# Performance work log

Hardware: AMD Instinct MI355X
Metric: run time of the kernel (lower is better)

The kernel has to match this reference:

```python
import jax, jax.numpy as jnp
import numpy as np
from jax import lax

B = 16   # batch
A = 40   # num_attributes

def _conv(x, w, b, pad):
    y = lax.conv_general_dilated(x, w, (1, 1), [(pad, pad), (pad, pad)],
                                 dimension_numbers=('NCHW', 'OIHW', 'NCHW'))
    return y + b[None, :, None, None]

def _bn_relu(y):
    # BatchNorm2d in training mode; gamma=1, beta=0 (the module's init values)
    m = y.mean(axis=(0, 2, 3), keepdims=True)
    v = ((y - m) ** 2).mean(axis=(0, 2, 3), keepdims=True)
    return jax.nn.relu((y - m) * lax.rsqrt(v + 1e-5))

def _maxpool2(y):
    return lax.reduce_window(y, -jnp.inf, lax.max, (1, 1, 2, 2), (1, 1, 2, 2), 'VALID')

def _gsm(s, t):
    # gumbel_softmax(s, t) == softmax(s / t) along dim 1 (no noise in source)
    return jax.nn.softmax(s / t, axis=1)

def _branch_layer(xb, wa, ba, wb, bb, br, t):
    # xb: [P, B, Cin, H, W]; wa/wb: per-branch conv weights stacked on axis 0
    def one(x, wai, bai, wbi, bbi):
        y = _bn_relu(_conv(x, wai, bai, 1))
        y = _bn_relu(_conv(y, wbi, bbi, 1))
        return _maxpool2(y)
    xs = jax.vmap(one)(xb, wa, ba, wb, bb)       # [P, B, Cout, H/2, W/2]
    # branching_op (training=True): d = softmax(log(softmax(br/0.5)) / t)
    d = _gsm(jnp.log(_gsm(br, 0.5)), float(t))   # [Cnext, P]
    return jnp.einsum('np,pbchw->nbchw', d, xs)  # weighted sum over parents

def reference(x, w10, b10, wa0, ba0, wb0, bb0, wa1, ba1, wb1, bb1,
              wa2, ba2, wb2, bb2, wa3, ba3, wb3, bb3,
              br0, br1, br2, br3, fw1, fb1, fw2, fb2, fw3, fb3, t):
    y = _maxpool2(_bn_relu(_conv(x, w10, b10, 0)))   # conv1_0: [B,64,125,125]
    xb = jnp.stack([y, y])                           # x_branches = [x, x]
    for wa, ba, wb, bb, br in ((wa0, ba0, wb0, bb0, br0),
                               (wa1, ba1, wb1, bb1, br1),
                               (wa2, ba2, wb2, bb2, br2),
                               (wa3, ba3, wb3, bb3, br3)):
        xb = _branch_layer(xb, wa, ba, wb, bb, br, t)
    # xb: [A, B, 32, 7, 7]; AdaptiveAvgPool2d((7,7)) on 7x7 input is identity
    f = xb.reshape(A, B, -1)                          # [A, B, 1568]
    # per-attribute fc1/fc2 heads batched over the attribute axis (dropout omitted)
    h = jax.nn.relu(jnp.einsum('abf,afh->abh', f, fw1) + fb1[:, None, :])
    h = jax.nn.relu(jnp.einsum('abh,ahk->abk', h, fw2) + fb2[:, None, :])
    o = jnp.einsum('abh,ahk->abk', h, fw3) + fb3[:, None, :]   # [A, B, 1]
    return jnp.transpose(o[:, :, 0])                  # cat along dim 1 -> [B, A]

def setup_inputs():
    key = jax.random.key(0)
    ki = iter(jax.random.split(key, 64))
    def rn(shape, s):
        return jax.random.normal(next(ki), shape, jnp.float32) * s
    inp = {'x': jax.random.normal(next(ki), (B, 3, 256, 256), jnp.float32)}
    inp['w10'] = rn((64, 3, 7, 7), 0.1)
    inp['b10'] = jnp.zeros((64,), jnp.float32)
    P = [2, 4, 8, 16]       # parents per branch layer
    cout = [64, 64, 64, 32] # num_in_channels[layer+1]
    for L in range(4):
        inp['wa%d' % L] = rn((P[L], 64, 64, 3, 3), 0.06)
        inp['ba%d' % L] = jnp.zeros((P[L], 64), jnp.float32)
        inp['wb%d' % L] = rn((P[L], cout[L], 64, 3, 3), 0.06)
        inp['bb%d' % L] = jnp.zeros((P[L], cout[L]), jnp.float32)
    C = [4, 8, 16, A]       # children per branch layer
    for L in range(4):
        inp['br%d' % L] = jax.random.uniform(next(ki), (C[L], P[L]), dtype=jnp.float32)
    inp['fw1'] = rn((A, 1568, 128), 0.01)
    inp['fb1'] = jnp.zeros((A, 128), jnp.float32)
    inp['fw2'] = rn((A, 128, 128), 0.01)
    inp['fb2'] = jnp.zeros((A, 128), jnp.float32)
    inp['fw3'] = rn((A, 128, 1), 0.01)
    inp['fb3'] = jnp.zeros((A, 1), jnp.float32)
    inp['t'] = 10
    return inp
```

## Files before the change

### kernel.cpp

```cpp
#include <hip/hip_runtime.h>
#include <math.h>

#define DIVUP(a,b) (((a)+(b)-1)/(b))

typedef _Float16 f16x8 __attribute__((ext_vector_type(8)));
typedef _Float16 f16x4 __attribute__((ext_vector_type(4)));
typedef float    f32x4 __attribute__((ext_vector_type(4)));

#define LBAR() do { asm volatile("s_waitcnt lgkmcnt(0)" ::: "memory"); \
                    __builtin_amdgcn_s_barrier(); } while (0)

template<int POOL, int C1, int HinP, int WinP, int Hout, int Wout, int Cout,
         int M, int NITER, int H2, int W2, int H2c, int W2c>
__global__ __launch_bounds__(256, 4) void conv_mfma(
    const _Float16* __restrict__ in, long inZstride,
    const _Float16* __restrict__ wt,
    float* __restrict__ out, long outZstride, float2* __restrict__ part)
{
    __shared__ __align__(16) char smem[10240];
    float2* red = (float2*)smem;

    int bx;
    {
        int n = gridDim.x, orig = blockIdx.x;
        int q = n >> 3, r = n & 7;
        int xcd = orig & 7, idx = orig >> 3;
        bx = (xcd < r ? xcd * (q + 1) : r * (q + 1) + (xcd - r) * q) + idx;
    }

    const int tid  = threadIdx.x;
    const int wv   = tid >> 6;
    const int ln15 = tid & 15;
    const int lhi  = (tid >> 4) & 3;
    const int sn   = tid & 63;
    const int skb  = tid >> 6;
    const int sdst = sn * 40 + skb * 8;

    const _Float16* ip = in + (size_t)blockIdx.z * inZstride;

    auto pixbase = [&](int mA) -> int {
        int nb, h, w; bool valid;
        if (POOL) {
            int r = mA & 3, quad = mA >> 2;
            const int cpi = H2c * W2c;
            nb = quad / cpi;
            int rem = quad - nb * cpi;
            int h2 = rem / W2c, w2 = rem - h2 * W2c;
            h = h2 * 2 + (r >> 1); w = w2 * 2 + (r & 1);
            valid = (mA < M) && (h < Hout) && (w < Wout);
        } else {
            const int HW = Hout * Wout;
            valid = mA < M;
            int mm = valid ? mA : 0;
            nb = mm / HW;
            int rem = mm - nb * HW;
            h = rem / Wout; w = rem - h * Wout;
        }
        if (!valid) { nb = 0; h = 0; w = 0; }
        if (C1) return ((nb * 256 + h) * 256 + w) * 4;
        return ((nb * HinP + h) * WinP + w) * 64;
    };
    auto rowvalid = [&](int mA) -> bool {
        if (POOL) {
            int r = mA & 3, quad = mA >> 2;
            const int cpi = H2c * W2c;
            int nb = quad / cpi;
            int rem = quad - nb * cpi;
            int h2 = rem / W2c, w2 = rem - h2 * W2c;
            int h = h2 * 2 + (r >> 1), w = w2 * 2 + (r & 1);
            return (mA < M) && (h < Hout) && (w < Wout);
        }
        return mA < M;
    };

    int abase[2];
#pragma unroll
    for (int q = 0; q < 2; ++q)
        abase[q] = pixbase(bx * 128 + wv * 32 + q * 16 + ln15);

    unsigned vmask = 0;
#pragma unroll
    for (int q = 0; q < 2; ++q)
#pragma unroll
        for (int r = 0; r < 4; ++r)
            vmask |= (unsigned)rowvalid(bx * 128 + wv * 32 + q * 16 + lhi * 4 + r)
                     << (q * 4 + r);

    const _Float16* wp = wt + (size_t)blockIdx.z * NITER * 2048;

    auto loadA = [&](int it, f16x8 (&a)[2]) {
        int off;
        if (C1) off = it * 1024 + lhi * 8;
        else { int tap = it >> 1; int kh = tap / 3, kw = tap - 3 * kh;
               off = (kh * WinP + kw) * 64 + (it & 1) * 32 + lhi * 8; }
#pragma unroll
        for (int q = 0; q < 2; ++q)
            a[q] = *(const f16x8*)(ip + abase[q] + off);
    };

    f32x4 acc[2][4] = {};
    f16x8 a0[2], a1[2], a2[2];
    f16x8 sb;

    {
        f16x8 h = *(const f16x8*)(wp + (size_t)(skb * 64 + sn) * 8);
        *(f16x8*)((_Float16*)smem + sdst) = h;
        loadA(0, a0);
        if (NITER > 1) {
            loadA(1, a1);
            sb = *(const f16x8*)(wp + (size_t)((4 + skb) * 64 + sn) * 8);
        }
        if (NITER > 2) loadA(2, a2);
        LBAR();
    }

#define REGION(IT, CUR, AR)                                                       \
    {                                                                             \
        const int itc = (IT);                                                     \
        if (itc + 1 < NITER)                                                      \
            *(f16x8*)((_Float16*)(smem + ((CUR) ^ 1) * 5120) + sdst) = sb;        \
        const _Float16* rb = (const _Float16*)(smem + (CUR) * 5120);              \
        f16x8 bf[4];                                                              \
        _Pragma("unroll")                                                         \
        for (int t = 0; t < 4; ++t)                                               \
            bf[t] = *(const f16x8*)(rb + (t * 16 + ln15) * 40 + lhi * 8);         \
        if (itc + 2 < NITER)                                                      \
            sb = *(const f16x8*)(wp +                                             \
                     (size_t)(((itc + 2) * 4 + skb) * 64 + sn) * 8);              \
        _Pragma("unroll")                                                         \
        for (int t = 0; t < 4; ++t)                                               \
            _Pragma("unroll")                                                     \
            for (int q = 0; q < 2; ++q)                                           \
                acc[q][t] = __builtin_amdgcn_mfma_f32_16x16x32_f16(AR[q], bf[t], acc[q][t], 0, 0, 0); \
        if (itc + 3 < NITER) loadA(itc + 3, AR);                                  \
        LBAR();                                                                   \
    }

    for (int it = 0; it < NITER; it += 6) {
        REGION(it, 0, a0);
        if (it + 1 < NITER) REGION(it + 1, 1, a1);
        if (it + 2 < NITER) REGION(it + 2, 0, a2);
        if (it + 3 < NITER) REGION(it + 3, 1, a0);
        if (it + 4 < NITER) REGION(it + 4, 0, a1);
        if (it + 5 < NITER) REGION(it + 5, 1, a2);
    }
#undef REGION

#pragma unroll
    for (int t = 0; t < 4; ++t) {
        float s = 0.f, s2 = 0.f;
#pragma unroll
        for (int q = 0; q < 2; ++q)
#pragma unroll
            for (int r = 0; r < 4; ++r) {
                float v = ((vmask >> (q * 4 + r)) & 1u) ? acc[q][t][r] : 0.f;
                s += v; s2 += v * v;
            }
        red[(ln15 + 16 * t) * 17 + (wv * 4 + lhi)] = make_float2(s, s2);
    }
    __syncthreads();
    if (tid < 64) {
        float s = 0.f, s2 = 0.f;
#pragma unroll
        for (int q = 0; q < 16; ++q) { float2 v = red[tid * 17 + q]; s += v.x; s2 += v.y; }
        part[((size_t)blockIdx.z * 64 + tid) * gridDim.x + bx] = make_float2(s, s2);
    }

    float* zout = out + (size_t)blockIdx.z * outZstride;
#pragma unroll
    for (int q = 0; q < 2; ++q) {
        const int mbase = bx * 128 + wv * 32 + q * 16 + lhi * 4;
        if (POOL) {
            if (mbase < M) {
                int quad = mbase >> 2;
                const int cpi = H2c * W2c;
                int nb2  = quad / cpi;
                int rem  = quad - nb2 * cpi;
                int h2 = rem / W2c, w2 = rem - h2 * W2c;
                if (h2 < H2 && w2 < W2) {
                    float* op = zout + ((size_t)(nb2 * H2 + h2) * W2 + w2) * Cout;
#pragma unroll
                    for (int t = 0; t < 4; ++t) {
                        int n = ln15 + 16 * t;
                        if (n < Cout) {
                            float mx = fmaxf(fmaxf(acc[q][t][0], acc[q][t][1]),
                                             fmaxf(acc[q][t][2], acc[q][t][3]));
                            op[n] = mx;
                        }
                    }
                }
            }
        } else {
#pragma unroll
            for (int r = 0; r < 4; ++r) {
                int m = mbase + r;
                if (m < M) {
                    float* op = zout + (size_t)m * Cout;
#pragma unroll
                    for (int t = 0; t < 4; ++t) {
                        int n = ln15 + 16 * t;
                        if (n < Cout) op[n] = acc[q][t][r];
                    }
                }
            }
        }
    }
}

__global__ __launch_bounds__(256) void bn_finalize(const float2* __restrict__ part,
                                                   int nblkx, double Ninv,
                                                   float2* __restrict__ stats)
{
    __shared__ double sh[512];
    const int zc = blockIdx.x, tid = threadIdx.x;
    const float2* p = part + (size_t)zc * nblkx;
    double s = 0, s2 = 0;
    for (int i = tid; i < nblkx; i += 256) { s += p[i].x; s2 += p[i].y; }
    sh[tid] = s; sh[256 + tid] = s2;
    __syncthreads();
    for (int st = 128; st > 0; st >>= 1) {
        if (tid < st) { sh[tid] += sh[tid + st]; sh[256 + tid] += sh[256 + tid + st]; }
        __syncthreads();
    }
    if (tid == 0) {
        float mean = (float)(sh[0] * Ninv);
        float var  = (float)(sh[256] * Ninv - (double)mean * (double)mean);
        if (var < 0.f) var = 0.f;
        stats[zc] = make_float2(mean, rsqrtf(var + 1e-5f));
    }
}

__global__ void bn_split(const float* __restrict__ raw, const float2* __restrict__ stats,
                         _Float16* __restrict__ outF, int H, int W, int total)
{
    int idx = blockIdx.x * 256 + threadIdx.x;
    if (idx >= total) return;
    const int Hp = H + 2, Wp = W + 2;
    int c4 = idx & 15;
    int t  = idx >> 4;
    int wp = t % Wp; t /= Wp;
    int hp = t % Hp; int img = t / Hp;
    size_t o = (((size_t)img * Hp + hp) * Wp + wp) * 64 + c4 * 4;
    f16x4 hi;
    if (hp == 0 || hp == Hp - 1 || wp == 0 || wp == Wp - 1) {
#pragma unroll
        for (int j = 0; j < 4; ++j) hi[j] = (_Float16)0.f;
    } else {
        float4 v = *(const float4*)(raw + (((size_t)img * H + (hp - 1)) * W + (wp - 1)) * 64 + c4 * 4);
        const float2* st = stats + (img >> 4) * 64 + c4 * 4;
        float vv[4] = {v.x, v.y, v.z, v.w};
#pragma unroll
        for (int j = 0; j < 4; ++j) {
            float2 s = st[j];
            hi[j] = (_Float16)fmaxf((vv[j] - s.x) * s.y, 0.f);
        }
    }
    *(f16x4*)(outF + o) = hi;
}

__global__ void mix_split(const float* __restrict__ pooled, const float2* __restrict__ stats,
                          const float* __restrict__ d, _Float16* __restrict__ outF,
                          int H, int W, int P, long strideP, int total)
{
    int idx = blockIdx.x * 256 + threadIdx.x;
    if (idx >= total) return;
    const int Hp = H + 2, Wp = W + 2;
    int c4 = idx & 15;
    int t  = idx >> 4;
    int wp = t % Wp; t /= Wp;
    int hp = t % Hp; t /= Hp;
    int n  = t & 15;
    int cc = t >> 4;
    size_t o = (((size_t)(cc * 16 + n) * Hp + hp) * Wp + wp) * 64 + c4 * 4;
    f16x4 hi;
    if (hp == 0 || hp == Hp - 1 || wp == 0 || wp == Wp - 1) {
#pragma unroll
        for (int j = 0; j < 4; ++j) hi[j] = (_Float16)0.f;
    } else {
        float a[4] = {0.f, 0.f, 0.f, 0.f};
        const float* pb = pooled + (((size_t)n * H + (hp - 1)) * W + (wp - 1)) * 64 + c4 * 4;
        for (int p = 0; p < P; ++p) {
            float4 v = *(const float4*)(pb + (size_t)p * strideP);
            const float2* st = stats + p * 64 + c4 * 4;
            float dc = d[cc * P + p];
            float vv[4] = {v.x, v.y, v.z, v.w};
#pragma unroll
            for (int j = 0; j < 4; ++j) {
                float2 s = st[j];
                a[j] = fmaf(dc, fmaxf((vv[j] - s.x) * s.y, 0.f), a[j]);
            }
        }
#pragma unroll
        for (int j = 0; j < 4; ++j) hi[j] = (_Float16)a[j];
    }
    *(f16x4*)(outF + o) = hi;
}

__global__ void mix_last(const float* __restrict__ pooled, const float2* __restrict__ stats,
                         const float* __restrict__ d, float* __restrict__ out, int total)
{
    int idx = blockIdx.x * 256 + threadIdx.x;
    if (idx >= total) return;
    int c  = idx & 31;
    int t  = idx >> 5;
    int hw = t % 49; t /= 49;
    int n  = t & 15;
    int a  = t >> 4;
    float acc = 0.f;
    const float* pb = pooled + ((size_t)n * 49 + hw) * 32 + c;
    for (int p = 0; p < 16; ++p) {
        float2 s = stats[p * 64 + c];
        acc = fmaf(d[a * 16 + p], fmaxf((pb[(size_t)p * 25088] - s.x) * s.y, 0.f), acc);
    }
    out[idx] = acc;
}

__global__ void prep_x(const float* __restrict__ x, _Float16* __restrict__ xF)
{
    int idx = blockIdx.x * 256 + threadIdx.x;
    if (idx >= 16 * 65536) return;
    int n = idx >> 16, hw = idx & 65535;
    f16x4 hi;
#pragma unroll
    for (int ci = 0; ci < 3; ++ci)
        hi[ci] = (_Float16)x[((size_t)n * 3 + ci) * 65536 + hw];
    hi[3] = (_Float16)0.f;
    *(f16x4*)(xF + (size_t)idx * 4) = hi;
}

__global__ void wtrans1(const float* __restrict__ w, _Float16* __restrict__ wt)
{
    int i = blockIdx.x * 256 + threadIdx.x;
    if (i >= 28 * 512) return;
    int j = i & 7, n = (i >> 3) & 63, kb = i >> 9;
    int k = kb * 8 + j;
    int kh = k >> 5, r = k & 31, kw = r >> 2, ci = r & 3;
    float v = (kw < 7 && ci < 3) ? w[((n * 3 + ci) * 7 + kh) * 7 + kw] : 0.f;
    wt[i] = (_Float16)v;
}

__global__ void wtrans3(const float* __restrict__ w, _Float16* __restrict__ wt,
                        int P, int Cout)
{
    int total = P * 72 * 512;
    for (int i = blockIdx.x * 256 + threadIdx.x; i < total; i += gridDim.x * 256) {
        int j = i & 7, n = (i >> 3) & 63, kb = (i >> 9) % 72, p = (i >> 9) / 72;
        int k = kb * 8 + j;
        int ci = k & 63, tap = k >> 6, kh = tap / 3, kw = tap - 3 * kh;
        float v = (n < Cout) ? w[(((size_t)(p * Cout + n)) * 64 + ci) * 9 + kh * 3 + kw] : 0.f;
        wt[i] = (_Float16)v;
    }
}

__global__ void dcalc(const float* __restrict__ br0, const float* __restrict__ br1,
                      const float* __restrict__ br2, const float* __restrict__ br3,
                      const void* __restrict__ tptr, float* __restrict__ D)
{
    const int L = blockIdx.x;
    const float* br; int C, P, off;
    if      (L == 0) { br = br0; C = 4;  P = 2;  off = 0;   }
    else if (L == 1) { br = br1; C = 8;  P = 4;  off = 8;   }
    else if (L == 2) { br = br2; C = 16; P = 8;  off = 40;  }
    else             { br = br3; C = 40; P = 16; off = 168; }
    int ti = *(const int*)tptr;
    float t = (ti > 0 && ti < 1000000) ? (float)ti : *(const float*)tptr;
    const int c = threadIdx.x;
    if (c >= C) return;
    float u[16];
    float mx = -1e30f;
#pragma unroll
    for (int p = 0; p < 16; ++p) if (p < P) { u[p] = br[c * P + p] * 2.0f; mx = fmaxf(mx, u[p]); }
    float se = 0.f;
#pragma unroll
    for (int p = 0; p < 16; ++p) if (p < P) se += expf(u[p] - mx);
    float lse = mx + logf(se);
    float mx2 = -1e30f;
#pragma unroll
    for (int p = 0; p < 16; ++p) if (p < P) { u[p] = (u[p] - lse) / t; mx2 = fmaxf(mx2, u[p]); }
    float se2 = 0.f;
#pragma unroll
    for (int p = 0; p < 16; ++p) if (p < P) { u[p] = expf(u[p] - mx2); se2 += u[p]; }
#pragma unroll
    for (int p = 0; p < 16; ++p) if (p < P) D[off + c * P + p] = u[p] / se2;
}

__global__ __launch_bounds__(128) void fc1_k(const float* __restrict__ f,
                                             const float* __restrict__ w1,
                                             const float* __restrict__ b1,
                                             float* __restrict__ h1)
{
    const int a = blockIdx.x >> 4;
    const int b = blockIdx.x & 15;
    const int i = threadIdx.x;
    const float* fv = f + ((size_t)a * 16 + b) * 1568;
    const float* wv = w1 + (size_t)a * 1568 * 128 + i;
    float acc = b1[a * 128 + i];
    for (int hw = 0; hw < 49; ++hw)
        for (int c = 0; c < 32; ++c)
            acc = fmaf(fv[hw * 32 + c], wv[(size_t)(c * 49 + hw) * 128], acc);
    h1[((size_t)a * 16 + b) * 128 + i] = fmaxf(acc, 0.f);
}

__global__ __launch_bounds__(128) void fc23_k(const float* __restrict__ h1,
                                              const float* __restrict__ w2,
                                              const float* __restrict__ b2,
                                              const float* __restrict__ w3,
                                              const float* __restrict__ b3,
                                              float* __restrict__ out)
{
    __shared__ float sh1[16][128];
    __shared__ float sh2[16][128];
    const int a = blockIdx.x;
    const int i = threadIdx.x;
    for (int b = 0; b < 16; ++b) sh1[b][i] = h1[((size_t)a * 16 + b) * 128 + i];
    __syncthreads();
    float acc[16];
#pragma unroll
    for (int b = 0; b < 16; ++b) acc[b] = b2[a * 128 + i];
    for (int ff = 0; ff < 128; ++ff) {
        float wv = w2[((size_t)a * 128 + ff) * 128 + i];
#pragma unroll
        for (int b = 0; b < 16; ++b) acc[b] = fmaf(sh1[b][ff], wv, acc[b]);
    }
    for (int b = 0; b < 16; ++b) sh2[b][i] = fmaxf(acc[b], 0.f);
    __syncthreads();
    if (i < 16) {
        float o = b3[a];
        for (int ff = 0; ff < 128; ++ff) o = fmaf(sh2[i][ff], w3[a * 128 + ff], o);
        out[i * 40 + a] = o;
    }
}

extern "C" void kernel_launch(void* const* d_in, const int* in_sizes, int n_in,
                              void* d_out, int out_size, void* d_ws, size_t ws_size,
                              hipStream_t stream)
{
    (void)in_sizes; (void)n_in;

    const float* x   = (const float*)d_in[0];
    const float* w10 = (const float*)d_in[1];
    const float* wa[4] = {(const float*)d_in[3],  (const float*)d_in[7],
                          (const float*)d_in[11], (const float*)d_in[15]};
    const float* wb[4] = {(const float*)d_in[5],  (const float*)d_in[9],
                          (const float*)d_in[13], (const float*)d_in[17]};
    const float* br[4] = {(const float*)d_in[19], (const float*)d_in[20],
                          (const float*)d_in[21], (const float*)d_in[22]};
    const float* fw1 = (const float*)d_in[23];
    const float* fb1 = (const float*)d_in[24];
    const float* fw2 = (const float*)d_in[25];
    const float* fb2 = (const float*)d_in[26];
    const float* fw3 = (const float*)d_in[27];
    const float* fb3 = (const float*)d_in[28];
    float* out = (float*)d_out;

    const int Pl[4]  = {2, 4, 8, 16};
    const int CBs[4] = {64, 64, 64, 32};

    const size_t NEED = 42374400ull * 4ull;
    if (ws_size < NEED) {
        hipMemsetAsync(d_out, 0, (size_t)out_size * sizeof(float), stream);
        return;
    }
    float* ws = (float*)d_ws;
    size_t o = 0;
    _Float16* WT1 = (_Float16*)(ws + o); o += 7168;
    _Float16 *WTA[4], *WTB[4];
    for (int L = 0; L < 4; ++L) {
        WTA[L] = (_Float16*)(ws + o); o += (size_t)Pl[L] * 18432;
        WTB[L] = (_Float16*)(ws + o); o += (size_t)Pl[L] * 18432;
    }
    float*  D     = ws + o; o += 1024;
    float2* STATS = (float2*)(ws + o); o += 4352;
    float2* STATS_C1 = STATS;
    float2* STATS_A  = STATS + 64;
    float2* STATS_B  = STATS + 1088;
    float*  H1 = ws + o; o += 81920;
    float*  A6 = ws + o; o += 524288;
    float*  A5 = ws + o; o += 7872512;
    float*  A4 = ws + o; o += 16000000;
    float*  A3 = ws + o; o += 8388608;
    float*  A2 = ws + o; o += 8388608;

    float2* PART   = (float2*)A6;
    float2* PARTC1 = (float2*)A5;
    _Float16* xcF = (_Float16*)A3;
    _Float16* A2F = (_Float16*)A2;
    _Float16* A3F = (_Float16*)A3;

    prep_x<<<4096, 256, 0, stream>>>(x, xcF);
    wtrans1<<<56, 256, 0, stream>>>(w10, WT1);
    for (int L = 0; L < 4; ++L) {
        int tA = Pl[L] * 72 * 512;
        wtrans3<<<DIVUP(tA, 256), 256, 0, stream>>>(wa[L], WTA[L], Pl[L], 64);
        wtrans3<<<DIVUP(tA, 256), 256, 0, stream>>>(wb[L], WTB[L], Pl[L], CBs[L]);
    }
    dcalc<<<4, 64, 0, stream>>>(br[0], br[1], br[2], br[3], d_in[29], D);

    conv_mfma<1, 1, 256, 256, 250, 250, 64, 1000000, 7, 125, 125, 125, 125>
        <<<dim3(7813, 1, 1), 256, 0, stream>>>(xcF, 0, WT1, A4, 0, PARTC1);
    bn_finalize<<<64, 256, 0, stream>>>(PARTC1, 7813, 1.0 / 1000000.0, STATS_C1);
    bn_split<<<DIVUP(16 * 127 * 127 * 16, 256), 256, 0, stream>>>(
        A4, STATS_C1, A2F, 125, 125, 16 * 127 * 127 * 16);

    for (int p = 0; p < 2; ++p) {
        conv_mfma<0, 0, 127, 127, 125, 125, 64, 250000, 18, 0, 0, 1, 1>
            <<<dim3(1954, 1, 1), 256, 0, stream>>>(
                A2F, 0, WTA[0] + (size_t)p * 36864, A4, 0, PART);
        bn_finalize<<<64, 256, 0, stream>>>(PART, 1954, 1.0 / 250000.0, STATS_A);
        bn_split<<<DIVUP(16 * 127 * 127 * 16, 256), 256, 0, stream>>>(
            A4, STATS_A, A3F, 125, 125, 16 * 127 * 127 * 16);
        conv_mfma<1, 0, 127, 127, 125, 125, 64, 254016, 18, 62, 62, 63, 63>
            <<<dim3(1985, 1, 1), 256, 0, stream>>>(
                A3F, 0, WTB[0] + (size_t)p * 36864, A5 + (size_t)p * 3936256, 0, PART);
        bn_finalize<<<64, 256, 0, stream>>>(PART, 1985, 1.0 / 250000.0, STATS_B + p * 64);
    }
    mix_split<<<DIVUP(4 * 16 * 64 * 64 * 16, 256), 256, 0, stream>>>(
        A5, STATS_B, D + 0, A2F, 62, 62, 2, 3936256, 4 * 16 * 64 * 64 * 16);

    conv_mfma<0, 0, 64, 64, 62, 62, 64, 61504, 18, 0, 0, 1, 1>
        <<<dim3(481, 1, 4), 256, 0, stream>>>(
            A2F, 4194304, WTA[1], A4, 3936256, PART);
    bn_finalize<<<256, 256, 0, stream>>>(PART, 481, 1.0 / 61504.0, STATS_A);
    bn_split<<<DIVUP(64 * 64 * 64 * 16, 256), 256, 0, stream>>>(
        A4, STATS_A, A3F, 62, 62, 64 * 64 * 64 * 16);
    conv_mfma<1, 0, 64, 64, 62, 62, 64, 61504, 18, 31, 31, 31, 31>
        <<<dim3(481, 1, 4), 256, 0, stream>>>(
            A3F, 4194304, WTB[1], A5, 984064, PART);
    bn_finalize<<<256, 256, 0, stream>>>(PART, 481, 1.0 / 61504.0, STATS_B);
    mix_split<<<DIVUP(8 * 16 * 33 * 33 * 16, 256), 256, 0, stream>>>(
        A5, STATS_B, D + 8, A2F, 31, 31, 4, 984064, 8 * 16 * 33 * 33 * 16);

    conv_mfma<0, 0, 33, 33, 31, 31, 64, 15376, 18, 0, 0, 1, 1>
        <<<dim3(121, 1, 8), 256, 0, stream>>>(
            A2F, 1115136, WTA[2], A4, 984064, PART);
    bn_finalize<<<512, 256, 0, stream>>>(PART, 121, 1.0 / 15376.0, STATS_A);
    bn_split<<<DIVUP(128 * 33 * 33 * 16, 256), 256, 0, stream>>>(
        A4, STATS_A, A3F, 31, 31, 128 * 33 * 33 * 16);
    conv_mfma<1, 0, 33, 33, 31, 31, 64, 16384, 18, 15, 15, 16, 16>
        <<<dim3(128, 1, 8), 256, 0, stream>>>(
            A3F, 1115136, WTB[2], A5, 230400, PART);
    bn_finalize<<<512, 256, 0, stream>>>(PART, 128, 1.0 / 15376.0, STATS_B);
    mix_split<<<DIVUP(16 * 16 * 17 * 17 * 16, 256), 256, 0, stream>>>(
        A5, STATS_B, D + 40, A2F, 15, 15, 8, 230400, 16 * 16 * 17 * 17 * 16);

    conv_mfma<0, 0, 17, 17, 15, 15, 64, 3600, 18, 0, 0, 1, 1>
        <<<dim3(29, 1, 16), 256, 0, stream>>>(
            A2F, 295936, WTA[3], A4, 230400, PART);
    bn_finalize<<<1024, 256, 0, stream>>>(PART, 29, 1.0 / 3600.0, STATS_A);
    bn_split<<<DIVUP(256 * 17 * 17 * 16, 256), 256, 0, stream>>>(
        A4, STATS_A, A3F, 15, 15, 256 * 17 * 17 * 16);
    conv_mfma<1, 0, 17, 17, 15, 15, 32, 4096, 18, 7, 7, 8, 8>
        <<<dim3(32, 1, 16), 256, 0, stream>>>(
            A3F, 295936, WTB[3], A5, 25088, PART);
    bn_finalize<<<1024, 256, 0, stream>>>(PART, 32, 1.0 / 3600.0, STATS_B);
    mix_last<<<DIVUP(40 * 16 * 49 * 32, 256), 256, 0, stream>>>(
        A5, STATS_B, D + 168, A2, 40 * 16 * 49 * 32);

    fc1_k<<<640, 128, 0, stream>>>(A2, fw1, fb1, H1);
    fc23_k<<<40, 128, 0, stream>>>(H1, fw2, fb2, fw3, fb3, out);
}
```

Before: 678.1 us.

## Store conv outputs in fp16, batch first branch layer's parents, raise occupancy

Conv outputs (pre-BN activations and pooled results) are now written and read as fp16 rather than fp32, halving the traffic between conv kernels and the BN/mix kernels. The first branch layer's two parents are now launched together through the grid z dimension instead of a host loop, which cuts launch count and fills more of the GPU. Launch bounds are raised to 8 blocks per CU, and the workspace layout is resized to fit. Storing raw pre-normalisation values in fp16 risks small accuracy loss, and the tighter register budget could cause spills.

After: 1.766 ms. 2.6x slower.

```diff
diff --git a/kernel.cpp b/kernel.cpp
--- a/kernel.cpp
+++ b/kernel.cpp
@@ -12,10 +12,10 @@
 
 template<int POOL, int C1, int HinP, int WinP, int Hout, int Wout, int Cout,
          int M, int NITER, int H2, int W2, int H2c, int W2c>
-__global__ __launch_bounds__(256, 4) void conv_mfma(
+__global__ __launch_bounds__(256, 8) void conv_mfma(
     const _Float16* __restrict__ in, long inZstride,
     const _Float16* __restrict__ wt,
-    float* __restrict__ out, long outZstride, float2* __restrict__ part)
+    _Float16* __restrict__ out, long outZstride, float2* __restrict__ part)
 {
     __shared__ __align__(16) char smem[10240];
     float2* red = (float2*)smem;
@@ -166,7 +166,7 @@
         part[((size_t)blockIdx.z * 64 + tid) * gridDim.x + bx] = make_float2(s, s2);
     }
 
-    float* zout = out + (size_t)blockIdx.z * outZstride;
+    _Float16* zout = out + (size_t)blockIdx.z * outZstride;
 #pragma unroll
     for (int q = 0; q < 2; ++q) {
         const int mbase = bx * 128 + wv * 32 + q * 16 + lhi * 4;
@@ -178,14 +178,14 @@
                 int rem  = quad - nb2 * cpi;
                 int h2 = rem / W2c, w2 = rem - h2 * W2c;
                 if (h2 < H2 && w2 < W2) {
-                    float* op = zout + ((size_t)(nb2 * H2 + h2) * W2 + w2) * Cout;
+                    _Float16* op = zout + ((size_t)(nb2 * H2 + h2) * W2 + w2) * Cout;
 #pragma unroll
                     for (int t = 0; t < 4; ++t) {
                         int n = ln15 + 16 * t;
                         if (n < Cout) {
                             float mx = fmaxf(fmaxf(acc[q][t][0], acc[q][t][1]),
                                              fmaxf(acc[q][t][2], acc[q][t][3]));
-                            op[n] = mx;
+                            op[n] = (_Float16)mx;
                         }
                     }
                 }
@@ -195,11 +195,11 @@
             for (int r = 0; r < 4; ++r) {
                 int m = mbase + r;
                 if (m < M) {
-                    float* op = zout + (size_t)m * Cout;
+                    _Float16* op = zout + (size_t)m * Cout;
 #pragma unroll
                     for (int t = 0; t < 4; ++t) {
                         int n = ln15 + 16 * t;
-                        if (n < Cout) op[n] = acc[q][t][r];
+                        if (n < Cout) op[n] = (_Float16)acc[q][t][r];
                     }
                 }
             }
@@ -230,7 +230,7 @@
     }
 }
 
-__global__ void bn_split(const float* __restrict__ raw, const float2* __restrict__ stats,
+__global__ void bn_split(const _Float16* __restrict__ raw, const float2* __restrict__ stats,
                          _Float16* __restrict__ outF, int H, int W, int total)
 {
     int idx = blockIdx.x * 256 + threadIdx.x;
@@ -246,19 +246,18 @@
 #pragma unroll
         for (int j = 0; j < 4; ++j) hi[j] = (_Float16)0.f;
     } else {
-        float4 v = *(const float4*)(raw + (((size_t)img * H + (hp - 1)) * W + (wp - 1)) * 64 + c4 * 4);
+        f16x4 v = *(const f16x4*)(raw + (((size_t)img * H + (hp - 1)) * W + (wp - 1)) * 64 + c4 * 4);
         const float2* st = stats + (img >> 4) * 64 + c4 * 4;
-        float vv[4] = {v.x, v.y, v.z, v.w};
 #pragma unroll
         for (int j = 0; j < 4; ++j) {
             float2 s = st[j];
-            hi[j] = (_Float16)fmaxf((vv[j] - s.x) * s.y, 0.f);
+            hi[j] = (_Float16)fmaxf(((float)v[j] - s.x) * s.y, 0.f);
         }
     }
     *(f16x4*)(outF + o) = hi;
 }
 
-__global__ void mix_split(const float* __restrict__ pooled, const float2* __restrict__ stats,
+__global__ void mix_split(const _Float16* __restrict__ pooled, const float2* __restrict__ stats,
                           const float* __restrict__ d, _Float16* __restrict__ outF,
                           int H, int W, int P, long strideP, int total)
 {
@@ -278,16 +277,15 @@
         for (int j = 0; j < 4; ++j) hi[j] = (_Float16)0.f;
     } else {
         float a[4] = {0.f, 0.f, 0.f, 0.f};
-        const float* pb = pooled + (((size_t)n * H + (hp - 1)) * W + (wp - 1)) * 64 + c4 * 4;
+        const _Float16* pb = pooled + (((size_t)n * H + (hp - 1)) * W + (wp - 1)) * 64 + c4 * 4;
         for (int p = 0; p < P; ++p) {
-            float4 v = *(const float4*)(pb + (size_t)p * strideP);
+            f16x4 v = *(const f16x4*)(pb + (size_t)p * strideP);
             const float2* st = stats + p * 64 + c4 * 4;
             float dc = d[cc * P + p];
-            float vv[4] = {v.x, v.y, v.z, v.w};
 #pragma unroll
             for (int j = 0; j < 4; ++j) {
                 float2 s = st[j];
-                a[j] = fmaf(dc, fmaxf((vv[j] - s.x) * s.y, 0.f), a[j]);
+                a[j] = fmaf(dc, fmaxf(((float)v[j] - s.x) * s.y, 0.f), a[j]);
             }
         }
 #pragma unroll
@@ -296,7 +294,7 @@
     *(f16x4*)(outF + o) = hi;
 }
 
-__global__ void mix_last(const float* __restrict__ pooled, const float2* __restrict__ stats,
+__global__ void mix_last(const _Float16* __restrict__ pooled, const float2* __restrict__ stats,
                          const float* __restrict__ d, float* __restrict__ out, int total)
 {
     int idx = blockIdx.x * 256 + threadIdx.x;
@@ -307,10 +305,10 @@
     int n  = t & 15;
     int a  = t >> 4;
     float acc = 0.f;
-    const float* pb = pooled + ((size_t)n * 49 + hw) * 32 + c;
+    const _Float16* pb = pooled + ((size_t)n * 49 + hw) * 32 + c;
     for (int p = 0; p < 16; ++p) {
         float2 s = stats[p * 64 + c];
-        acc = fmaf(d[a * 16 + p], fmaxf((pb[(size_t)p * 25088] - s.x) * s.y, 0.f), acc);
+        acc = fmaf(d[a * 16 + p], fmaxf(((float)pb[(size_t)p * 25088] - s.x) * s.y, 0.f), acc);
     }
     out[idx] = acc;
 }
@@ -456,7 +454,7 @@
     const int Pl[4]  = {2, 4, 8, 16};
     const int CBs[4] = {64, 64, 64, 32};
 
-    const size_t NEED = 42374400ull * 4ull;
+    const size_t NEED = 47000000ull * 4ull;
     if (ws_size < NEED) {
         hipMemsetAsync(d_out, 0, (size_t)out_size * sizeof(float), stream);
         return;
@@ -476,16 +474,18 @@
     float2* STATS_B  = STATS + 1088;
     float*  H1 = ws + o; o += 81920;
     float*  A6 = ws + o; o += 524288;
-    float*  A5 = ws + o; o += 7872512;
+    float*  A5 = ws + o; o += 4000000;
     float*  A4 = ws + o; o += 16000000;
-    float*  A3 = ws + o; o += 8388608;
-    float*  A2 = ws + o; o += 8388608;
+    float*  A3 = ws + o; o += 16600000;
+    float*  A2 = ws + o; o += 8400000;
 
     float2* PART   = (float2*)A6;
     float2* PARTC1 = (float2*)A5;
     _Float16* xcF = (_Float16*)A3;
     _Float16* A2F = (_Float16*)A2;
     _Float16* A3F = (_Float16*)A3;
+    _Float16* A4F = (_Float16*)A4;
+    _Float16* A5F = (_Float16*)A5;
 
     prep_x<<<4096, 256, 0, stream>>>(x, xcF);
     wtrans1<<<56, 256, 0, stream>>>(w10, WT1);
@@ -497,64 +497,62 @@
     dcalc<<<4, 64, 0, stream>>>(br[0], br[1], br[2], br[3], d_in[29], D);
 
     conv_mfma<1, 1, 256, 256, 250, 250, 64, 1000000, 7, 125, 125, 125, 125>
-        <<<dim3(7813, 1, 1), 256, 0, stream>>>(xcF, 0, WT1, A4, 0, PARTC1);
+        <<<dim3(7813, 1, 1), 256, 0, stream>>>(xcF, 0, WT1, A4F, 0, PARTC1);
     bn_finalize<<<64, 256, 0, stream>>>(PARTC1, 7813, 1.0 / 1000000.0, STATS_C1);
     bn_split<<<DIVUP(16 * 127 * 127 * 16, 256), 256, 0, stream>>>(
-        A4, STATS_C1, A2F, 125, 125, 16 * 127 * 127 * 16);
-
-    for (int p = 0; p < 2; ++p) {
-        conv_mfma<0, 0, 127, 127, 125, 125, 64, 250000, 18, 0, 0, 1, 1>
-            <<<dim3(1954, 1, 1), 256, 0, stream>>>(
-                A2F, 0, WTA[0] + (size_t)p * 36864, A4, 0, PART);
-        bn_finalize<<<64, 256, 0, stream>>>(PART, 1954, 1.0 / 250000.0, STATS_A);
-        bn_split<<<DIVUP(16 * 127 * 127 * 16, 256), 256, 0, stream>>>(
-            A4, STATS_A, A3F, 125, 125, 16 * 127 * 127 * 16);
-        conv_mfma<1, 0, 127, 127, 125, 125, 64, 254016, 18, 62, 62, 63, 63>
-            <<<dim3(1985, 1, 1), 256, 0, stream>>>(
-                A3F, 0, WTB[0] + (size_t)p * 36864, A5 + (size_t)p * 3936256, 0, PART);
-        bn_finalize<<<64, 256, 0, stream>>>(PART, 1985, 1.0 / 250000.0, STATS_B + p * 64);
-    }
+        A4F, STATS_C1, A2F, 125, 125, 16 * 127 * 127 * 16);
+
+    conv_mfma<0, 0, 127, 127, 125, 125, 64, 250000, 18, 0, 0, 1, 1>
+        <<<dim3(1954, 1, 2), 256, 0, stream>>>(
+            A2F, 0, WTA[0], A4F, 16000000, PART);
+    bn_finalize<<<128, 256, 0, stream>>>(PART, 1954, 1.0 / 250000.0, STATS_A);
+    bn_split<<<DIVUP(2 * 16 * 127 * 127 * 16, 256), 256, 0, stream>>>(
+        A4F, STATS_A, A3F, 125, 125, 2 * 16 * 127 * 127 * 16);
+    conv_mfma<1, 0, 127, 127, 125, 125, 64, 254016, 18, 62, 62, 63, 63>
+        <<<dim3(1985, 1, 2), 256, 0, stream>>>(
+            A3F, 16516096, WTB[0], A5F, 3936256, PART);
+    bn_finalize<<<128, 256, 0, stream>>>(PART, 1985, 1.0 / 250000.0, STATS_B);
     mix_split<<<DIVUP(4 * 16 * 64 * 64 * 16, 256), 256, 0, stream>>>(
-        A5, STATS_B, D + 0, A2F, 62, 62, 2, 3936256, 4 * 16 * 64 * 64 * 16);
+        A5F, STATS_B, D + 0, A2F, 62, 62, 2, 3936256, 4 * 16 * 64 * 64 * 16);
 
     conv_mfma<0, 0, 64, 64, 62, 62, 64, 61504, 18, 0, 0, 1, 1>
         <<<dim3(481, 1, 4), 256, 0, stream>>>(
-            A2F, 4194304, WTA[1], A4, 3936256, PART);
+            A2F, 4194304, WTA[1], A4F, 3936256, PART);
     bn_finalize<<<256, 256, 0, stream>>>(PART, 481, 1.0 / 61504.0, STATS_A);
     bn_split<<<DIVUP(64 * 64 * 64 * 16, 256), 256, 0, stream>>>(
-        A4, STATS_A, A3F, 62, 62, 64 * 64 * 64 * 16);
+        A4F, STATS_A, A3F, 62, 62, 64 * 64 * 64 * 16);
     conv_mfma<1, 0, 64, 64, 62, 62, 64, 61504, 18, 31, 31, 31, 31>
         <<<dim3(481, 1, 4), 256, 0, stream>>>(
-            A3F, 4194304, WTB[1], A5, 984064, PART);
+            A3F, 4194304, WTB[1], A5F, 984064, PART);
     bn_finalize<<<256, 256, 0, stream>>>(PART, 481, 1.0 / 61504.0, STATS_B);
     mix_split<<<DIVUP(8 * 16 * 33 * 33 * 16, 256), 256, 0, stream>>>(
-        A5, STATS_B, D + 8, A2F, 31, 31, 4, 984064, 8 * 16 * 33 * 33 * 16);
+        A5F, STATS_B, D + 8, A2F, 31, 31, 4, 984064, 8 * 16 * 33 * 33 * 16);
 
     conv_mfma<0, 0, 33, 33, 31, 31, 64, 15376, 18, 0, 0, 1, 1>
         <<<dim3(121, 1, 8), 256, 0, stream>>>(
-            A2F, 1115136, WTA[2], A4, 984064, PART);
+            A2F, 1115136, WTA[2], A4F, 984064, PART);
     bn_finalize<<<512, 256, 0, stream>>>(PART, 121, 1.0 / 15376.0, STATS_A);
     bn_split<<<DIVUP(128 * 33 * 33 * 16, 256), 256, 0, stream>>>(
-        A4, STATS_A, A3F, 31, 31, 128 * 33 * 33 * 16);
+        A4F, STATS_A, A3F, 31, 31, 128 * 33 * 33 * 16);
     conv_mfma<1, 0, 33, 33, 31, 31, 64, 16384, 18, 15, 15, 16, 16>
         <<<dim3(128, 1, 8), 256, 0, stream>>>(
-            A3F, 1115136, WTB[2], A5, 230400, PART);
+            A3F, 1115136, WTB[2], A5F, 230400, PART);
     bn_finalize<<<512, 256, 0, stream>>>(PART, 128, 1.0 / 15376.0, STATS_B);
     mix_split<<<DIVUP(16 * 16 * 17 * 17 * 16, 256), 256, 0, stream>>>(
-        A5, STATS_B, D + 40, A2F, 15, 15, 8, 230400, 16 * 16 * 17 * 17 * 16);
+        A5F, STATS_B, D + 40, A2F, 15, 15, 8, 230400, 16 * 16 * 17 * 17 * 16);
 
     conv_mfma<0, 0, 17, 17, 15, 15, 64, 3600, 18, 0, 0, 1, 1>
         <<<dim3(29, 1, 16), 256, 0, stream>>>(
-            A2F, 295936, WTA[3], A4, 230400, PART);
+            A2F, 295936, WTA[3], A4F, 230400, PART);
     bn_finalize<<<1024, 256, 0, stream>>>(PART, 29, 1.0 / 3600.0, STATS_A);
     bn_split<<<DIVUP(256 * 17 * 17 * 16, 256), 256, 0, stream>>>(
-        A4, STATS_A, A3F, 15, 15, 256 * 17 * 17 * 16);
+        A4F, STATS_A, A3F, 15, 15, 256 * 17 * 17 * 16);
     conv_mfma<1, 0, 17, 17, 15, 15, 32, 4096, 18, 7, 7, 8, 8>
         <<<dim3(32, 1, 16), 256, 0, stream>>>(
-            A3F, 295936, WTB[3], A5, 25088, PART);
+            A3F, 295936, WTB[3], A5F, 25088, PART);
     bn_finalize<<<1024, 256, 0, stream>>>(PART, 32, 1.0 / 3600.0, STATS_B);
     mix_last<<<DIVUP(40 * 16 * 49 * 32, 256), 256, 0, stream>>>(
-        A5, STATS_B, D + 168, A2, 40 * 16 * 49 * 32);
+        A5F, STATS_B, D + 168, A2, 40 * 16 * 49 * 32);
 
     fc1_k<<<640, 128, 0, stream>>>(A2, fw1, fb1, H1);
     fc23_k<<<40, 128, 0, stream>>>(H1, fw2, fb2, fw3, fb3, out);
```
